# Performance work log

Hardware: AMD Instinct MI355X
Metric: run time of the kernel (lower is better)

The kernel has to match this reference:

```python
import jax, jax.numpy as jnp
import numpy as np

B, L, D = 2, 1024, 768
H, DH = 12, 64
DP = 32
MLP = 4 * D
NL = 4
WINDOW = 128
EPS_RMS = 1.1920929e-07  # torch F.rms_norm default eps = finfo(float32).eps
EPS_LN = 1e-5


def rmsnorm(x):
    return x * jax.lax.rsqrt(jnp.mean(x * x, axis=-1, keepdims=True) + EPS_RMS)


def layernorm(x, g, b):
    m = jnp.mean(x, axis=-1, keepdims=True)
    v = jnp.mean((x - m) ** 2, axis=-1, keepdims=True)
    return (x - m) * jax.lax.rsqrt(v + EPS_LN) * g + b


def rope(q, k):
    # q,k: [B,H,L,DH]; standard rotate-half RoPE, theta=10000
    half = DH // 2
    inv_freq = 1.0 / (10000.0 ** (jnp.arange(0, DH, 2, dtype=jnp.float32) / DH))  # [half]
    freqs = jnp.arange(L, dtype=jnp.float32)[:, None] * inv_freq[None, :]  # [L,half]
    cos = jnp.concatenate([jnp.cos(freqs), jnp.cos(freqs)], -1)[None, None]  # [1,1,L,DH]
    sin = jnp.concatenate([jnp.sin(freqs), jnp.sin(freqs)], -1)[None, None]

    def rot(x):
        x1, x2 = jnp.split(x, 2, axis=-1)
        return jnp.concatenate([-x2, x1], axis=-1)

    return q * cos + rot(q) * sin, k * cos + rot(k) * sin


def setup_inputs() -> dict:
    key = jax.random.key(0)
    ks = jax.random.split(key, 16)
    sc = 0.02
    return {
        "s": jax.random.normal(ks[0], (B, L, D), jnp.float32),
        "pair": jax.random.normal(ks[1], (B, L, L, DP), jnp.float32),
        "qkv_w": jax.random.normal(ks[2], (NL, 3 * D, D), jnp.float32) * sc,
        "qkv_b": jnp.zeros((NL, 3 * D), jnp.float32),
        "out_w": jax.random.normal(ks[3], (NL, D, D), jnp.float32) * sc,
        "out_b": jnp.zeros((NL, D), jnp.float32),
        "fc1_w": jax.random.normal(ks[4], (NL, MLP, D), jnp.float32) * sc,
        "fc1_b": jnp.zeros((NL, MLP), jnp.float32),
        "fc2_w": jax.random.normal(ks[5], (NL, D, MLP), jnp.float32) * sc,
        "fc2_b": jnp.zeros((NL, D), jnp.float32),
        "ln_g": jnp.ones((NL, DP), jnp.float32),
        "ln_b": jnp.zeros((NL, DP), jnp.float32),
        "pb_w": jax.random.normal(ks[6], (NL, DP), jnp.float32) * sc,
        "pb_b": jnp.zeros((NL,), jnp.float32),
    }


def reference(s, pair, qkv_w, qkv_b, out_w, out_b, fc1_w, fc1_b, fc2_w, fc2_b,
              ln_g, ln_b, pb_w, pb_b):
    idx = jnp.arange(L)
    window_mask = jnp.abs(idx[:, None] - idx[None, :]) <= WINDOW  # [L,L]
    neg_inf = jnp.float32(-1e30)
    scale = 1.0 / jnp.sqrt(jnp.float32(DH))

    for l in range(NL):
        # pair bias score-mod: LayerNorm + Linear(DP,1)
        bias = layernorm(pair, ln_g[l], ln_b[l]) @ pb_w[l] + pb_b[l]  # [B,L,L]

        h = rmsnorm(s)
        qkv = h @ qkv_w[l].T + qkv_b[l]  # [B,L,3D]
        q, k, v = jnp.split(qkv, 3, axis=-1)
        q = q.reshape(B, L, H, DH).transpose(0, 2, 1, 3)
        k = k.reshape(B, L, H, DH).transpose(0, 2, 1, 3)
        v = v.reshape(B, L, H, DH).transpose(0, 2, 1, 3)
        q, k = rope(q, k)

        scores = jnp.einsum("bhqd,bhkd->bhqk", q, k) * scale + bias[:, None]
        scores = jnp.where(window_mask[None, None], scores, neg_inf)
        attn = jax.nn.softmax(scores, axis=-1)
        y = jnp.einsum("bhqk,bhkd->bhqd", attn, v)
        y = y.transpose(0, 2, 1, 3).reshape(B, L, D)
        s = s + y @ out_w[l].T + out_b[l]

        h = rmsnorm(s)
        h = jax.nn.gelu(h @ fc1_w[l].T + fc1_b[l], approximate=False)
        s = s + h @ fc2_w[l].T + fc2_b[l]
    return s
```

## Files before the change

kernel.cpp:

```cpp
#include <hip/hip_runtime.h>

#define B_    2
#define L_    1024
#define D_    768
#define H_    12
#define DH_   64
#define DP_   32
#define MLP_  3072
#define NL_   4
#define WIN_  128
#define W2_   257
#define M_    (B_*L_)

typedef __attribute__((ext_vector_type(8))) short bf16x8;
typedef __attribute__((ext_vector_type(4))) float f32x4;

__device__ __forceinline__ unsigned short f2bf(float x){
  unsigned int u = __float_as_uint(x);
  u += 0x7fffu + ((u >> 16) & 1u);
  return (unsigned short)(u >> 16);
}

__device__ __forceinline__ void gl_lds16(const void* g, void* l){
  __builtin_amdgcn_global_load_lds((__attribute__((address_space(1))) void*)g,
                                   (__attribute__((address_space(3))) void*)l, 16, 0, 0);
}

__global__ __launch_bounds__(256) void cvt_bf16_k(const float* __restrict__ src,
                                                  unsigned short* __restrict__ dst, int n4){
  int i = blockIdx.x*256 + threadIdx.x;
  if (i >= n4) return;
  float4 v = ((const float4*)src)[i];
  ushort4 o;
  o.x = f2bf(v.x); o.y = f2bf(v.y); o.z = f2bf(v.z); o.w = f2bf(v.w);
  ((ushort4*)dst)[i] = o;
}

__global__ __launch_bounds__(256) void pair_bias_k(const float* __restrict__ pair,
    const float* __restrict__ ln_g, const float* __restrict__ ln_b,
    const float* __restrict__ pb_w, const float* __restrict__ pb_b,
    float* __restrict__ bias){
  __shared__ float gw[NL_][DP_];
  __shared__ float cb[NL_];
  int tid = threadIdx.x;
  if (tid < NL_*DP_) gw[tid>>5][tid&31] = ln_g[tid]*pb_w[tid];
  if (tid < NL_){
    float c = 0.f;
    for (int d=0; d<DP_; ++d) c += ln_b[tid*DP_+d]*pb_w[tid*DP_+d];
    cb[tid] = c + pb_b[tid];
  }
  __syncthreads();
  int idx = blockIdx.x*256 + tid;
  if (idx >= B_*L_*W2_) return;
  int rel = idx % W2_;
  int t   = idx / W2_;
  int i   = t & (L_-1);
  int b   = t >> 10;
  int j   = i + rel - WIN_;
  if (j < 0 || j >= L_) return;
  const float4* p = (const float4*)(pair + ((size_t)(b*L_ + i)*L_ + j)*DP_);
  float4 x[8];
  #pragma unroll
  for (int q=0;q<8;++q) x[q] = p[q];
  float s=0.f, ss=0.f;
  #pragma unroll
  for (int q=0;q<8;++q){
    s  += x[q].x + x[q].y + x[q].z + x[q].w;
    ss += x[q].x*x[q].x + x[q].y*x[q].y + x[q].z*x[q].z + x[q].w*x[q].w;
  }
  float m  = s * (1.0f/DP_);
  float rs = rsqrtf(ss*(1.0f/DP_) - m*m + 1e-5f);
  #pragma unroll
  for (int l=0;l<NL_;++l){
    float acc = 0.f;
    #pragma unroll
    for (int q=0;q<8;++q){
      acc += (x[q].x-m)*gw[l][4*q+0] + (x[q].y-m)*gw[l][4*q+1]
           + (x[q].z-m)*gw[l][4*q+2] + (x[q].w-m)*gw[l][4*q+3];
    }
    bias[(((size_t)l*B_ + b)*L_ + i)*W2_ + rel] = acc*rs + cb[l];
  }
}

__global__ __launch_bounds__(256) void rmsnorm_k(const float* __restrict__ s,
                                                 unsigned short* __restrict__ h){
  int row = blockIdx.x, tid = threadIdx.x;
  const float* x = s + (size_t)row*D_;
  float v0 = x[tid], v1 = x[tid+256], v2 = x[tid+512];
  float ss = v0*v0 + v1*v1 + v2*v2;
  #pragma unroll
  for (int m=1; m<64; m<<=1) ss += __shfl_xor(ss, m, 64);
  __shared__ float wsum[4];
  __shared__ float rbuf;
  if ((tid & 63) == 0) wsum[tid>>6] = ss;
  __syncthreads();
  if (tid == 0) rbuf = rsqrtf((wsum[0]+wsum[1]+wsum[2]+wsum[3])*(1.0f/D_) + 1.1920929e-07f);
  __syncthreads();
  float r = rbuf;
  unsigned short* o = h + (size_t)row*D_;
  o[tid]     = f2bf(v0*r);
  o[tid+256] = f2bf(v1*r);
  o[tid+512] = f2bf(v2*r);
}

template<int MODE, int TM, int SPLIT>
__global__ __launch_bounds__(256) void gemm_bt(const unsigned short* __restrict__ A,
    const unsigned short* __restrict__ W, const float* __restrict__ bias,
    float* __restrict__ outf, unsigned short* __restrict__ outb,
    float* __restrict__ resid, int N, int K){
  constexpr int MI = TM/32;
  __shared__ __align__(16) short sm[2][(TM+128)*32];
  const int tid  = threadIdx.x;
  const int wave = tid >> 6, lane = tid & 63;
  const int m0 = blockIdx.y*TM, n0 = blockIdx.x << 7;
  const int KB = K / SPLIT;
  const int kbase = blockIdx.z * KB;
  const int wm = (wave >> 1)*(TM/2), wn = (wave & 1) << 6;
  const int lrow = lane & 15, ko = (lane >> 4) << 3;
  f32x4 acc[MI][4] = {};
  const unsigned short* Ag = A + (size_t)(m0 + (tid>>2))*K + kbase + ((tid&3)<<3);
  const unsigned short* Wg = W + (size_t)(n0 + (tid>>2))*K + kbase + ((tid&3)<<3);
  const size_t hstep = (size_t)64*K;
  const int nk = KB >> 5;
  {
    short* As = sm[0]; short* Bs = sm[0] + TM*32;
    gl_lds16(Ag, &As[tid*8]);
    if (TM == 128) gl_lds16(Ag + hstep, &As[(tid+256)*8]);
    gl_lds16(Wg, &Bs[tid*8]);
    gl_lds16(Wg + hstep, &Bs[(tid+256)*8]);
  }
  for (int it = 0; it < nk; ++it){
    __syncthreads();
    if (it + 1 < nk){
      short* As = sm[(it&1)^1]; short* Bs = As + TM*32;
      const int kt = (it+1) << 5;
      gl_lds16(Ag + kt, &As[tid*8]);
      if (TM == 128) gl_lds16(Ag + hstep + kt, &As[(tid+256)*8]);
      gl_lds16(Wg + kt, &Bs[tid*8]);
      gl_lds16(Wg + hstep + kt, &Bs[(tid+256)*8]);
    }
    const short* As = sm[it&1]; const short* Bs = As + TM*32;
    bf16x8 af[MI], bv[4];
    #pragma unroll
    for (int i=0;i<MI;++i) af[i] = *(const bf16x8*)&As[((wm + i*16 + lrow) << 5) + ko];
    #pragma unroll
    for (int i=0;i<4;++i)  bv[i] = *(const bf16x8*)&Bs[((wn + i*16 + lrow) << 5) + ko];
    #pragma unroll
    for (int mi=0;mi<MI;++mi)
      #pragma unroll
      for (int ni=0;ni<4;++ni)
        acc[mi][ni] = __builtin_amdgcn_mfma_f32_16x16x32_bf16(af[mi], bv[ni], acc[mi][ni], 0, 0, 0);
  }
  #pragma unroll
  for (int ni=0;ni<4;++ni){
    const int col = n0 + wn + ni*16 + lrow;
    const float bb = (SPLIT == 1 || blockIdx.z == 0) ? bias[col] : 0.f;
    #pragma unroll
    for (int mi=0;mi<MI;++mi){
      const int rw = m0 + wm + mi*16 + ((lane >> 4) << 2);
      #pragma unroll
      for (int r=0;r<4;++r){
        float v = acc[mi][ni][r] + bb;
        if (MODE == 0){
          outf[(size_t)(rw + r)*N + col] = v;
        } else if (MODE == 2){
          float g = 0.5f * v * (1.0f + erff(v * 0.70710678118654752f));
          outb[(size_t)(rw + r)*N + col] = f2bf(g);
        } else {
          if (SPLIT == 1) resid[(size_t)(rw + r)*D_ + col] += v;
          else            atomicAdd(&resid[(size_t)(rw + r)*D_ + col], v);
        }
      }
    }
  }
}

__global__ __launch_bounds__(256) void rope_k(const float* __restrict__ qkv,
    float* __restrict__ qr, float* __restrict__ kr){
  int idx = blockIdx.x*256 + threadIdx.x;
  int d  = idx & 63;
  int r  = idx >> 6;
  int i  = r & (L_-1);
  int bh = r >> 10;
  int b  = bh / H_, h = bh - (bh / H_)*H_;
  const float* base = qkv + ((size_t)(b*L_ + i))*(3*D_) + h*64 + d;
  float qv = base[0], kv = base[D_];
  int t = d & 31;
  float invf = expf(-(float)t * 0.28782313662425572f);
  float ang = (float)i * invf;
  float sn, cs;
  sincosf(ang, &sn, &cs);
  float pq = (d < 32) ? -base[32]    : base[-32];
  float pk = (d < 32) ? -base[D_+32] : base[D_-32];
  qr[idx] = qv*cs + pq*sn;
  kr[idx] = kv*cs + pk*sn;
}

__global__ __launch_bounds__(256) void attn_k(const float* __restrict__ qr,
    const float* __restrict__ kr, const float* __restrict__ qkvf,
    const float* __restrict__ bias, unsigned short* __restrict__ ybf, int layer){
  __shared__ __align__(16) short kb[288*72];
  __shared__ __align__(16) float sc[16*304];
  short* ps = (short*)sc;
  const int tid  = threadIdx.x;
  const int wave = tid >> 6, lane = tid & 63;
  const int quad = lane >> 4, lrow = lane & 15;
  const int bh = blockIdx.y, b = bh / H_, h = bh - b*H_;
  const int i0 = blockIdx.x * 16, jb = i0 - WIN_;

  bf16x8 qf0, qf1;
  {
    const float* qrow = qr + ((size_t)bh*L_ + i0 + lrow)*64 + quad*8;
    #pragma unroll
    for (int j=0;j<8;++j) qf0[j] = (short)f2bf(qrow[j]);
    #pragma unroll
    for (int j=0;j<8;++j) qf1[j] = (short)f2bf(qrow[32+j]);
  }
  {
    const int seg = tid & 3;
    for (int r = tid>>2; r < 288; r += 64){
      int jg = jb + r;
      short* dst = &kb[r*72 + seg*16];
      if (jg >= 0 && jg < L_){
        const float4* sp = (const float4*)(kr + ((size_t)bh*L_ + jg)*64 + seg*16);
        #pragma unroll
        for (int i=0;i<4;++i){
          float4 x = sp[i];
          short o0 = (short)f2bf(x.x), o1 = (short)f2bf(x.y);
          short o2 = (short)f2bf(x.z), o3 = (short)f2bf(x.w);
          dst[i*4+0]=o0; dst[i*4+1]=o1; dst[i*4+2]=o2; dst[i*4+3]=o3;
        }
      } else {
        #pragma unroll
        for (int i=0;i<16;++i) dst[i] = 0;
      }
    }
  }
  __syncthreads();
  for (int c = wave; c < 18; c += 4){
    const int krow = c*16 + lrow;
    bf16x8 kf0 = *(const bf16x8*)&kb[krow*72 + quad*8];
    bf16x8 kf1 = *(const bf16x8*)&kb[krow*72 + 32 + quad*8];
    f32x4 z = {0.f,0.f,0.f,0.f};
    f32x4 cc = __builtin_amdgcn_mfma_f32_16x16x32_bf16(qf0, kf0, z, 0, 0, 0);
    cc = __builtin_amdgcn_mfma_f32_16x16x32_bf16(qf1, kf1, cc, 0, 0, 0);
    const int jj = c*16 + lrow, jg = jb + jj;
    #pragma unroll
    for (int r=0;r<4;++r){
      const int row = quad*4 + r;
      const int rel = jj - row;
      float v = -1e30f;
      if (rel >= 0 && rel <= 256 && jg >= 0 && jg < L_)
        v = cc[r]*0.125f + bias[(((size_t)(layer*B_ + b))*L_ + i0 + row)*W2_ + rel];
      sc[row*304 + jj] = v;
    }
  }
  __syncthreads();
  const int qq = tid >> 4, tj = tid & 15;
  float ev[18];
  #pragma unroll
  for (int c=0;c<18;++c) ev[c] = sc[qq*304 + c*16 + tj];
  __syncthreads();
  float mx = -3.0e38f;
  #pragma unroll
  for (int c=0;c<18;++c) mx = fmaxf(mx, ev[c]);
  #pragma unroll
  for (int m=1; m<16; m<<=1) mx = fmaxf(mx, __shfl_xor(mx, m, 16));
  float sm = 0.f;
  #pragma unroll
  for (int c=0;c<18;++c){ float e = __expf(ev[c] - mx); ev[c] = e; sm += e; }
  #pragma unroll
  for (int m=1; m<16; m<<=1) sm += __shfl_xor(sm, m, 16);
  const float inv = 1.0f / sm;
  #pragma unroll
  for (int c=0;c<18;++c) ps[qq*288 + c*16 + tj] = (short)f2bf(ev[c]*inv);
  {
    const int seg = tid & 3;
    for (int r = tid>>2; r < 288; r += 64){
      int jg = jb + r;
      short* dst = &kb[r*72 + seg*16];
      if (jg >= 0 && jg < L_){
        const float4* sp = (const float4*)(qkvf + ((size_t)(b*L_ + jg))*2304 + 1536 + h*64 + seg*16);
        #pragma unroll
        for (int i=0;i<4;++i){
          float4 x = sp[i];
          short o0 = (short)f2bf(x.x), o1 = (short)f2bf(x.y);
          short o2 = (short)f2bf(x.z), o3 = (short)f2bf(x.w);
          dst[i*4+0]=o0; dst[i*4+1]=o1; dst[i*4+2]=o2; dst[i*4+3]=o3;
        }
      } else {
        #pragma unroll
        for (int i=0;i<16;++i) dst[i] = 0;
      }
    }
  }
  __syncthreads();
  f32x4 o = {0.f,0.f,0.f,0.f};
  for (int kc=0; kc<9; ++kc){
    bf16x8 af = *(const bf16x8*)&ps[lrow*288 + kc*32 + quad*8];
    bf16x8 bf;
    #pragma unroll
    for (int j=0;j<8;++j) bf[j] = kb[(kc*32 + quad*8 + j)*72 + wave*16 + lrow];
    o = __builtin_amdgcn_mfma_f32_16x16x32_bf16(af, bf, o, 0, 0, 0);
  }
  #pragma unroll
  for (int r=0;r<4;++r){
    const int row = quad*4 + r;
    ybf[((size_t)(b*L_ + i0 + row))*D_ + h*64 + wave*16 + lrow] = f2bf(o[r]);
  }
}

extern "C" void kernel_launch(void* const* d_in, const int* in_sizes, int n_in,
                              void* d_out, int out_size, void* d_ws, size_t ws_size,
                              hipStream_t stream){
  (void)in_sizes; (void)n_in; (void)out_size; (void)ws_size;
  const float* s_in  = (const float*)d_in[0];
  const float* pair  = (const float*)d_in[1];
  const float* qkv_w = (const float*)d_in[2];
  const float* qkv_b = (const float*)d_in[3];
  const float* out_w = (const float*)d_in[4];
  const float* out_b = (const float*)d_in[5];
  const float* fc1_w = (const float*)d_in[6];
  const float* fc1_b = (const float*)d_in[7];
  const float* fc2_w = (const float*)d_in[8];
  const float* fc2_b = (const float*)d_in[9];
  const float* ln_g  = (const float*)d_in[10];
  const float* ln_b  = (const float*)d_in[11];
  const float* pb_w  = (const float*)d_in[12];
  const float* pb_b  = (const float*)d_in[13];
  float* s = (float*)d_out;

  char* ws = (char*)d_ws;
  size_t off = 0;
  auto take = [&](size_t bytes)->char*{
    char* p = ws + off; off += (bytes + 255) & ~(size_t)255; return p;
  };
  unsigned short* wqkv = (unsigned short*)take((size_t)NL_*3*D_*D_*2);
  unsigned short* wout = (unsigned short*)take((size_t)NL_*D_*D_*2);
  unsigned short* wfc1 = (unsigned short*)take((size_t)NL_*MLP_*D_*2);
  unsigned short* wfc2 = (unsigned short*)take((size_t)NL_*D_*MLP_*2);
  float*          bw   = (float*)take((size_t)NL_*B_*L_*W2_*4);
  unsigned short* hbf  = (unsigned short*)take((size_t)M_*D_*2);
  float*          qkvf = (float*)take((size_t)M_*3*D_*4);
  float*          q_r  = (float*)take((size_t)B_*H_*L_*DH_*4);
  float*          k_r  = (float*)take((size_t)B_*H_*L_*DH_*4);
  unsigned short* ybf  = (unsigned short*)take((size_t)M_*D_*2);
  unsigned short* gbf  = (unsigned short*)take((size_t)M_*MLP_*2);

  hipMemcpyAsync(s, s_in, (size_t)M_*D_*sizeof(float), hipMemcpyDeviceToDevice, stream);

  auto cvt = [&](const float* src, unsigned short* dst, size_t n){
    int n4 = (int)(n/4);
    cvt_bf16_k<<<(n4+255)/256, 256, 0, stream>>>(src, dst, n4);
  };
  cvt(qkv_w, wqkv, (size_t)NL_*3*D_*D_);
  cvt(out_w, wout, (size_t)NL_*D_*D_);
  cvt(fc1_w, wfc1, (size_t)NL_*MLP_*D_);
  cvt(fc2_w, wfc2, (size_t)NL_*D_*MLP_);

  pair_bias_k<<<(B_*L_*W2_ + 255)/256, 256, 0, stream>>>(pair, ln_g, ln_b, pb_w, pb_b, bw);

  for (int l=0; l<NL_; ++l){
    rmsnorm_k<<<M_, 256, 0, stream>>>(s, hbf);
    gemm_bt<0,128,1><<<dim3((3*D_)/128, M_/128), 256, 0, stream>>>(
        hbf, wqkv + (size_t)l*3*D_*D_, qkv_b + l*3*D_, qkvf, nullptr, nullptr, 3*D_, D_);
    rope_k<<<(B_*H_*L_*DH_)/256, 256, 0, stream>>>(qkvf, q_r, k_r);
    attn_k<<<dim3(L_/16, B_*H_), 256, 0, stream>>>(q_r, k_r, qkvf, bw, ybf, l);
    gemm_bt<1,64,2><<<dim3(D_/128, M_/64, 2), 256, 0, stream>>>(
        ybf, wout + (size_t)l*D_*D_, out_b + l*D_, nullptr, nullptr, s, D_, D_);
    rmsnorm_k<<<M_, 256, 0, stream>>>(s, hbf);
    gemm_bt<2,128,1><<<dim3(MLP_/128, M_/128), 256, 0, stream>>>(
        hbf, wfc1 + (size_t)l*MLP_*D_, fc1_b + l*MLP_, nullptr, gbf, nullptr, MLP_, D_);
    gemm_bt<3,64,4><<<dim3(D_/128, M_/64, 4), 256, 0, stream>>>(
        gbf, wfc2 + (size_t)l*D_*MLP_, fc2_b + l*D_, nullptr, nullptr, s, D_, MLP_);
  }
}
```

Measured before the change: 1.037 ms.

## Store Q/K/V as head-major bf16 and double query rows per attention block

The QKV GEMM epilogue now writes V directly as head-major bf16, and rope emits bf16 Q and K, so the attention kernel loads 16-byte bf16 vectors instead of converting fp32 on the fly. Each attention block now handles 32 query rows instead of 16, so every staged K/V window of 288 rows is reused across twice as many queries and redundant window loads are halved. The cost is a larger score buffer in LDS and half as many blocks in the grid, which may lower occupancy.

```diff
diff --git a/kernel.cpp b/kernel.cpp
--- a/kernel.cpp
+++ b/kernel.cpp
@@ -162,7 +162,14 @@
       for (int r=0;r<4;++r){
         float v = acc[mi][ni][r] + bb;
         if (MODE == 0){
-          outf[(size_t)(rw + r)*N + col] = v;
+          if (col < 2*D_){
+            outf[(size_t)(rw + r)*N + col] = v;
+          } else {
+            const int rowg = rw + r;
+            const int bI = rowg >> 10, jI = rowg & (L_-1);
+            const int hI = (col - 2*D_) >> 6;
+            outb[(((size_t)(bI*H_ + hI)*L_ + jI) << 6) + (col & 63)] = f2bf(v);
+          }
         } else if (MODE == 2){
           float g = 0.5f * v * (1.0f + erff(v * 0.70710678118654752f));
           outb[(size_t)(rw + r)*N + col] = f2bf(g);
@@ -176,7 +183,7 @@
 }
 
 __global__ __launch_bounds__(256) void rope_k(const float* __restrict__ qkv,
-    float* __restrict__ qr, float* __restrict__ kr){
+    unsigned short* __restrict__ qr, unsigned short* __restrict__ kr){
   int idx = blockIdx.x*256 + threadIdx.x;
   int d  = idx & 63;
   int r  = idx >> 6;
@@ -192,121 +199,117 @@
   sincosf(ang, &sn, &cs);
   float pq = (d < 32) ? -base[32]    : base[-32];
   float pk = (d < 32) ? -base[D_+32] : base[D_-32];
-  qr[idx] = qv*cs + pq*sn;
-  kr[idx] = kv*cs + pk*sn;
-}
-
-__global__ __launch_bounds__(256) void attn_k(const float* __restrict__ qr,
-    const float* __restrict__ kr, const float* __restrict__ qkvf,
+  qr[idx] = f2bf(qv*cs + pq*sn);
+  kr[idx] = f2bf(kv*cs + pk*sn);
+}
+
+__global__ __launch_bounds__(256) void attn_k(const unsigned short* __restrict__ qr,
+    const unsigned short* __restrict__ kr, const unsigned short* __restrict__ vr,
     const float* __restrict__ bias, unsigned short* __restrict__ ybf, int layer){
   __shared__ __align__(16) short kb[288*72];
-  __shared__ __align__(16) float sc[16*304];
+  __shared__ __align__(16) float sc[32*304];
   short* ps = (short*)sc;
   const int tid  = threadIdx.x;
   const int wave = tid >> 6, lane = tid & 63;
   const int quad = lane >> 4, lrow = lane & 15;
   const int bh = blockIdx.y, b = bh / H_, h = bh - b*H_;
-  const int i0 = blockIdx.x * 16, jb = i0 - WIN_;
-
-  bf16x8 qf0, qf1;
+  const int i0 = blockIdx.x * 32, jb = i0 - WIN_;
+
+  bf16x8 qf[2][2];
+  #pragma unroll
+  for (int mt=0; mt<2; ++mt){
+    const unsigned short* qrow = qr + (((size_t)bh*L_ + i0 + mt*16 + lrow) << 6) + quad*8;
+    qf[mt][0] = *(const bf16x8*)qrow;
+    qf[mt][1] = *(const bf16x8*)(qrow + 32);
+  }
   {
-    const float* qrow = qr + ((size_t)bh*L_ + i0 + lrow)*64 + quad*8;
-    #pragma unroll
-    for (int j=0;j<8;++j) qf0[j] = (short)f2bf(qrow[j]);
-    #pragma unroll
-    for (int j=0;j<8;++j) qf1[j] = (short)f2bf(qrow[32+j]);
-  }
-  {
-    const int seg = tid & 3;
-    for (int r = tid>>2; r < 288; r += 64){
-      int jg = jb + r;
-      short* dst = &kb[r*72 + seg*16];
-      if (jg >= 0 && jg < L_){
-        const float4* sp = (const float4*)(kr + ((size_t)bh*L_ + jg)*64 + seg*16);
-        #pragma unroll
-        for (int i=0;i<4;++i){
-          float4 x = sp[i];
-          short o0 = (short)f2bf(x.x), o1 = (short)f2bf(x.y);
-          short o2 = (short)f2bf(x.z), o3 = (short)f2bf(x.w);
-          dst[i*4+0]=o0; dst[i*4+1]=o1; dst[i*4+2]=o2; dst[i*4+3]=o3;
-        }
-      } else {
-        #pragma unroll
-        for (int i=0;i<16;++i) dst[i] = 0;
-      }
+    const int r0 = tid >> 3, seg = tid & 7;
+    #pragma unroll
+    for (int p=0; p<9; ++p){
+      const int r = r0 + p*32;
+      const int jg = jb + r;
+      bf16x8 z;
+      #pragma unroll
+      for (int q=0;q<8;++q) z[q] = 0;
+      if ((unsigned)jg < L_) z = *(const bf16x8*)(kr + (((size_t)bh*L_ + jg) << 6) + seg*8);
+      *(bf16x8*)&kb[r*72 + seg*8] = z;
     }
   }
   __syncthreads();
   for (int c = wave; c < 18; c += 4){
     const int krow = c*16 + lrow;
-    bf16x8 kf0 = *(const bf16x8*)&kb[krow*72 + quad*8];
-    bf16x8 kf1 = *(const bf16x8*)&kb[krow*72 + 32 + quad*8];
-    f32x4 z = {0.f,0.f,0.f,0.f};
-    f32x4 cc = __builtin_amdgcn_mfma_f32_16x16x32_bf16(qf0, kf0, z, 0, 0, 0);
-    cc = __builtin_amdgcn_mfma_f32_16x16x32_bf16(qf1, kf1, cc, 0, 0, 0);
+    const bf16x8 kf0 = *(const bf16x8*)&kb[krow*72 + quad*8];
+    const bf16x8 kf1 = *(const bf16x8*)&kb[krow*72 + 32 + quad*8];
     const int jj = c*16 + lrow, jg = jb + jj;
     #pragma unroll
-    for (int r=0;r<4;++r){
-      const int row = quad*4 + r;
-      const int rel = jj - row;
-      float v = -1e30f;
-      if (rel >= 0 && rel <= 256 && jg >= 0 && jg < L_)
-        v = cc[r]*0.125f + bias[(((size_t)(layer*B_ + b))*L_ + i0 + row)*W2_ + rel];
-      sc[row*304 + jj] = v;
+    for (int mt=0; mt<2; ++mt){
+      f32x4 cc = {0.f,0.f,0.f,0.f};
+      cc = __builtin_amdgcn_mfma_f32_16x16x32_bf16(qf[mt][0], kf0, cc, 0, 0, 0);
+      cc = __builtin_amdgcn_mfma_f32_16x16x32_bf16(qf[mt][1], kf1, cc, 0, 0, 0);
+      #pragma unroll
+      for (int r=0;r<4;++r){
+        const int row = mt*16 + quad*4 + r;
+        const int rel = jj - row;
+        float v = -1e30f;
+        if (rel >= 0 && rel <= 256 && (unsigned)jg < L_)
+          v = cc[r]*0.125f + bias[(((size_t)(layer*B_ + b))*L_ + i0 + row)*W2_ + rel];
+        sc[row*304 + jj] = v;
+      }
     }
   }
   __syncthreads();
   const int qq = tid >> 4, tj = tid & 15;
-  float ev[18];
-  #pragma unroll
-  for (int c=0;c<18;++c) ev[c] = sc[qq*304 + c*16 + tj];
-  __syncthreads();
-  float mx = -3.0e38f;
-  #pragma unroll
-  for (int c=0;c<18;++c) mx = fmaxf(mx, ev[c]);
-  #pragma unroll
-  for (int m=1; m<16; m<<=1) mx = fmaxf(mx, __shfl_xor(mx, m, 16));
-  float sm = 0.f;
-  #pragma unroll
-  for (int c=0;c<18;++c){ float e = __expf(ev[c] - mx); ev[c] = e; sm += e; }
-  #pragma unroll
-  for (int m=1; m<16; m<<=1) sm += __shfl_xor(sm, m, 16);
-  const float inv = 1.0f / sm;
-  #pragma unroll
-  for (int c=0;c<18;++c) ps[qq*288 + c*16 + tj] = (short)f2bf(ev[c]*inv);
+  float ev[2][18];
+  #pragma unroll
+  for (int g=0; g<2; ++g)
+    #pragma unroll
+    for (int c=0;c<18;++c) ev[g][c] = sc[(qq + g*16)*304 + c*16 + tj];
+  __syncthreads();
+  #pragma unroll
+  for (int g=0; g<2; ++g){
+    float mx = -3.0e38f;
+    #pragma unroll
+    for (int c=0;c<18;++c) mx = fmaxf(mx, ev[g][c]);
+    #pragma unroll
+    for (int m=1; m<16; m<<=1) mx = fmaxf(mx, __shfl_xor(mx, m, 16));
+    float sm = 0.f;
+    #pragma unroll
+    for (int c=0;c<18;++c){ float e = __expf(ev[g][c] - mx); ev[g][c] = e; sm += e; }
+    #pragma unroll
+    for (int m=1; m<16; m<<=1) sm += __shfl_xor(sm, m, 16);
+    const float inv = 1.0f / sm;
+    #pragma unroll
+    for (int c=0;c<18;++c) ps[(qq + g*16)*296 + c*16 + tj] = (short)f2bf(ev[g][c]*inv);
+  }
   {
-    const int seg = tid & 3;
-    for (int r = tid>>2; r < 288; r += 64){
-      int jg = jb + r;
-      short* dst = &kb[r*72 + seg*16];
-      if (jg >= 0 && jg < L_){
-        const float4* sp = (const float4*)(qkvf + ((size_t)(b*L_ + jg))*2304 + 1536 + h*64 + seg*16);
-        #pragma unroll
-        for (int i=0;i<4;++i){
-          float4 x = sp[i];
-          short o0 = (short)f2bf(x.x), o1 = (short)f2bf(x.y);
-          short o2 = (short)f2bf(x.z), o3 = (short)f2bf(x.w);
-          dst[i*4+0]=o0; dst[i*4+1]=o1; dst[i*4+2]=o2; dst[i*4+3]=o3;
-        }
-      } else {
-        #pragma unroll
-        for (int i=0;i<16;++i) dst[i] = 0;
-      }
-    }
-  }
-  __syncthreads();
-  f32x4 o = {0.f,0.f,0.f,0.f};
+    const int r0 = tid >> 3, seg = tid & 7;
+    #pragma unroll
+    for (int p=0; p<9; ++p){
+      const int r = r0 + p*32;
+      const int jg = jb + r;
+      bf16x8 z;
+      #pragma unroll
+      for (int q=0;q<8;++q) z[q] = 0;
+      if ((unsigned)jg < L_) z = *(const bf16x8*)(vr + (((size_t)bh*L_ + jg) << 6) + seg*8);
+      *(bf16x8*)&kb[r*72 + seg*8] = z;
+    }
+  }
+  __syncthreads();
+  f32x4 o0 = {0.f,0.f,0.f,0.f}, o1 = {0.f,0.f,0.f,0.f};
   for (int kc=0; kc<9; ++kc){
-    bf16x8 af = *(const bf16x8*)&ps[lrow*288 + kc*32 + quad*8];
     bf16x8 bf;
     #pragma unroll
     for (int j=0;j<8;++j) bf[j] = kb[(kc*32 + quad*8 + j)*72 + wave*16 + lrow];
-    o = __builtin_amdgcn_mfma_f32_16x16x32_bf16(af, bf, o, 0, 0, 0);
+    const bf16x8 a0 = *(const bf16x8*)&ps[lrow*296 + kc*32 + quad*8];
+    const bf16x8 a1 = *(const bf16x8*)&ps[(16 + lrow)*296 + kc*32 + quad*8];
+    o0 = __builtin_amdgcn_mfma_f32_16x16x32_bf16(a0, bf, o0, 0, 0, 0);
+    o1 = __builtin_amdgcn_mfma_f32_16x16x32_bf16(a1, bf, o1, 0, 0, 0);
   }
   #pragma unroll
   for (int r=0;r<4;++r){
     const int row = quad*4 + r;
-    ybf[((size_t)(b*L_ + i0 + row))*D_ + h*64 + wave*16 + lrow] = f2bf(o[r]);
+    ybf[((size_t)(b*L_ + i0 + row))*D_ + h*64 + wave*16 + lrow]      = f2bf(o0[r]);
+    ybf[((size_t)(b*L_ + i0 + 16 + row))*D_ + h*64 + wave*16 + lrow] = f2bf(o1[r]);
   }
 }
 
@@ -342,8 +345,9 @@
   float*          bw   = (float*)take((size_t)NL_*B_*L_*W2_*4);
   unsigned short* hbf  = (unsigned short*)take((size_t)M_*D_*2);
   float*          qkvf = (float*)take((size_t)M_*3*D_*4);
-  float*          q_r  = (float*)take((size_t)B_*H_*L_*DH_*4);
-  float*          k_r  = (float*)take((size_t)B_*H_*L_*DH_*4);
+  unsigned short* qrb  = (unsigned short*)take((size_t)B_*H_*L_*DH_*2);
+  unsigned short* krb  = (unsigned short*)take((size_t)B_*H_*L_*DH_*2);
+  unsigned short* vrb  = (unsigned short*)take((size_t)B_*H_*L_*DH_*2);
   unsigned short* ybf  = (unsigned short*)take((size_t)M_*D_*2);
   unsigned short* gbf  = (unsigned short*)take((size_t)M_*MLP_*2);
 
@@ -363,9 +367,9 @@
   for (int l=0; l<NL_; ++l){
     rmsnorm_k<<<M_, 256, 0, stream>>>(s, hbf);
     gemm_bt<0,128,1><<<dim3((3*D_)/128, M_/128), 256, 0, stream>>>(
-        hbf, wqkv + (size_t)l*3*D_*D_, qkv_b + l*3*D_, qkvf, nullptr, nullptr, 3*D_, D_);
-    rope_k<<<(B_*H_*L_*DH_)/256, 256, 0, stream>>>(qkvf, q_r, k_r);
-    attn_k<<<dim3(L_/16, B_*H_), 256, 0, stream>>>(q_r, k_r, qkvf, bw, ybf, l);
+        hbf, wqkv + (size_t)l*3*D_*D_, qkv_b + l*3*D_, qkvf, vrb, nullptr, 3*D_, D_);
+    rope_k<<<(B_*H_*L_*DH_)/256, 256, 0, stream>>>(qkvf, qrb, krb);
+    attn_k<<<dim3(L_/32, B_*H_), 256, 0, stream>>>(qrb, krb, vrb, bw, ybf, l);
     gemm_bt<1,64,2><<<dim3(D_/128, M_/64, 2), 256, 0, stream>>>(
         ybf, wout + (size_t)l*D_*D_, out_b + l*D_, nullptr, nullptr, s, D_, D_);
     rmsnorm_k<<<M_, 256, 0, stream>>>(s, hbf);
```

Measured after the change: 1.021 ms. No clear change (-1.6%).
